# Kernel optimization log

Measured on AMD Instinct MI355X. Metric: run time of the kernel, lower is better.

## Reference

```python
import jax, jax.numpy as jnp
import numpy as np

H = 1024          # hidden_size
D = 4             # num_domains
B, S = 8, 2048


def setup_inputs() -> dict:
    key = jax.random.key(0)
    ks = jax.random.split(key, 12)
    inp = {
        "sequence_embeddings": jax.random.normal(ks[0], (B, S, H), jnp.float32),
        "volatility": jax.random.uniform(ks[1], (B, S, 1), jnp.float32) * 0.02 + 0.005,
        "risk_factors": jax.random.normal(ks[2], (B, S, 1), jnp.float32) * 0.01,
        # learned parameters (match torch init scales)
        "domain_feature_weights": jax.random.normal(ks[3], (H, 2 * H), jnp.float32) * 0.02,
        "domain_feature_bias": jnp.zeros((2 * H,), jnp.float32),
        "domain_classifier_weights": jax.random.normal(ks[4], (2 * H, D), jnp.float32) * 0.02,
        "domain_classifier_bias": jnp.zeros((D,), jnp.float32),
        "volatility_router_weights": jax.random.normal(ks[5], (1, 8, D), jnp.float32) * 0.1,
        "volatility_router_bias": jnp.zeros((8, D), jnp.float32),
        "risk_router_weights": jax.random.normal(ks[6], (1, 8, D), jnp.float32) * 0.1,
        "risk_router_bias": jnp.zeros((8, D), jnp.float32),
        "stats_router_weights": jax.random.normal(ks[7], (3, 12, D), jnp.float32) * 0.1,
        "stats_router_bias": jnp.zeros((12, D), jnp.float32),
        "expert_weights": jax.random.normal(ks[8], (D, 2 * H, H), jnp.float32) * 0.02,
        "expert_bias": jnp.zeros((D, H), jnp.float32),
    }
    return inp


def reference(sequence_embeddings, volatility, risk_factors,
              domain_feature_weights, domain_feature_bias,
              domain_classifier_weights, domain_classifier_bias,
              volatility_router_weights, volatility_router_bias,
              risk_router_weights, risk_router_bias,
              stats_router_weights, stats_router_bias,
              expert_weights, expert_bias):
    x = sequence_embeddings
    # shared domain feature extractor: [B,S,H] -> [B,S,2H]
    feat = jnp.tanh(jnp.einsum('bsh,hf->bsf', x, domain_feature_weights) + domain_feature_bias)
    # content-based domain logits [B,S,D]
    dom_logits = jnp.einsum('bsf,fd->bsd', feat, domain_classifier_weights) + domain_classifier_bias
    # volatility router: scalar -> 8 hidden units per domain, tanh, sum -> [B,S,D]
    vol_logits = jnp.tanh(volatility[..., None] * volatility_router_weights[0]
                          + volatility_router_bias).sum(axis=-2)
    # risk router, same structure
    risk_logits = jnp.tanh(risk_factors[..., None] * risk_router_weights[0]
                           + risk_router_bias).sum(axis=-2)
    # per-token statistics (mean/std/max over feature dim) -> [B,S,3]
    stats = jnp.stack([x.mean(axis=-1), x.std(axis=-1), x.max(axis=-1)], axis=-1)
    stats_logits = jnp.tanh(jnp.einsum('bsc,ckd->bskd', stats, stats_router_weights)
                            + stats_router_bias).sum(axis=-2)
    # combined routing distribution over domains
    routing_probs = jax.nn.softmax(dom_logits + vol_logits + risk_logits + stats_logits, axis=-1)
    # dispatch every token through all D experts: [B,S,D,H]
    expert_out = jnp.einsum('bsf,dfh->bsdh', feat, expert_weights) + expert_bias
    # gated combine: [B,S,H]
    out = jnp.einsum('bsd,bsdh->bsh', routing_probs, expert_out)
    return out
```

## Files before the change

kernel.cpp:

```cpp
#include <hip/hip_runtime.h>
#include <hip/hip_bf16.h>
#include <cstdint>
#include <cstddef>

typedef __bf16 bf16_t;
typedef bf16_t bf16x8 __attribute__((ext_vector_type(8)));
typedef bf16_t bf16x4 __attribute__((ext_vector_type(4)));
typedef float  f32x4  __attribute__((ext_vector_type(4)));
typedef int    i32x4  __attribute__((ext_vector_type(4)));

#define TOK 16384
#define Hh  1024
#define F2  2048
#define NC  4096

__device__ __forceinline__ void gload_lds16(const bf16_t* g, bf16_t* lds) {
  __builtin_amdgcn_global_load_lds(
      (const __attribute__((address_space(1))) void*)g,
      (__attribute__((address_space(3))) void*)lds, 16, 0, 0);
}
__device__ __forceinline__ void gload_lds16b(const int8_t* g, int8_t* lds) {
  __builtin_amdgcn_global_load_lds(
      (const __attribute__((address_space(1))) void*)g,
      (__attribute__((address_space(3))) void*)lds, 16, 0, 0);
}

__global__ __launch_bounds__(256)
void k_tr_wf(const float* __restrict__ in, bf16_t* __restrict__ out) {
  __shared__ float T[64][65];
  const int f0 = blockIdx.x * 64, h0 = blockIdx.y * 64;
  const int tid = threadIdx.x;
  const int c4 = (tid & 15) * 4, r = tid >> 4;
  #pragma unroll
  for (int p = 0; p < 4; ++p) {
    int hh = p * 16 + r;
    float4 v = *(const float4*)&in[(size_t)(h0 + hh) * F2 + f0 + c4];
    T[c4 + 0][hh] = v.x; T[c4 + 1][hh] = v.y; T[c4 + 2][hh] = v.z; T[c4 + 3][hh] = v.w;
  }
  __syncthreads();
  #pragma unroll
  for (int p = 0; p < 4; ++p) {
    int ff = p * 16 + r;
    bf16x4 o = { (bf16_t)T[ff][c4 + 0], (bf16_t)T[ff][c4 + 1],
                 (bf16_t)T[ff][c4 + 2], (bf16_t)T[ff][c4 + 3] };
    *(bf16x4*)&out[(size_t)(f0 + ff) * Hh + h0 + c4] = o;
  }
}

__global__ void k_we_scale1(const float* __restrict__ We, float* __restrict__ pmax) {
  int ht = blockIdx.x, fc = blockIdx.y, d = blockIdx.z;
  int h = ht * 256 + threadIdx.x;
  float m = 0.f;
  for (int ff = 0; ff < 256; ++ff) {
    float v = We[((size_t)d * F2 + fc * 256 + ff) * Hh + h];
    m = fmaxf(m, fabsf(v));
  }
  pmax[(size_t)(h * 4 + d) * 8 + fc] = m;
}
__global__ void k_we_scale2(const float* __restrict__ pmax, float* __restrict__ SB) {
  int cp = blockIdx.x * 256 + threadIdx.x;
  float m = 0.f;
  #pragma unroll
  for (int i = 0; i < 8; ++i) m = fmaxf(m, pmax[(size_t)cp * 8 + i]);
  SB[cp] = m;
}

__global__ __launch_bounds__(256)
void k_tr_we(const float* __restrict__ in, const float* __restrict__ SB,
             int8_t* __restrict__ out) {
  __shared__ float T[64][65];
  const int f0 = blockIdx.x * 64, h0 = blockIdx.y * 64, d = blockIdx.z;
  const float* ind = in + (size_t)d * F2 * Hh;
  const int tid = threadIdx.x;
  const int c4 = (tid & 15) * 4, r = tid >> 4;
  #pragma unroll
  for (int p = 0; p < 4; ++p) {
    int ff = p * 16 + r;
    float4 v = *(const float4*)&ind[(size_t)(f0 + ff) * Hh + h0 + c4];
    T[c4 + 0][ff] = v.x; T[c4 + 1][ff] = v.y; T[c4 + 2][ff] = v.z; T[c4 + 3][ff] = v.w;
  }
  __syncthreads();
  #pragma unroll
  for (int p = 0; p < 4; ++p) {
    int hh = p * 16 + r;
    int cp = (h0 + hh) * 4 + d;
    float m = SB[cp];
    float inv = (m > 1e-30f) ? 127.f / m : 0.f;
    char4 o;
    o.x = (int8_t)__float2int_rn(T[hh][c4 + 0] * inv);
    o.y = (int8_t)__float2int_rn(T[hh][c4 + 1] * inv);
    o.z = (int8_t)__float2int_rn(T[hh][c4 + 2] * inv);
    o.w = (int8_t)__float2int_rn(T[hh][c4 + 3] * inv);
    *(char4*)&out[(size_t)cp * F2 + f0 + c4] = o;
  }
}

__global__ void k_router_w(const float* __restrict__ x, const float* __restrict__ vol,
                           const float* __restrict__ risk, const float* __restrict__ clsb,
                           const float* __restrict__ vw, const float* __restrict__ vb,
                           const float* __restrict__ rw, const float* __restrict__ rb,
                           const float* __restrict__ sw, const float* __restrict__ sb,
                           bf16_t* __restrict__ xbf, float* __restrict__ LP,
                           int m0, int Tc) {
  int w = threadIdx.x >> 6, l = threadIdx.x & 63;
  int t = blockIdx.x * 4 + w;
  if (t >= Tc) return;
  int s = m0 + t;
  const float4* xr = (const float4*)(x + (size_t)s * Hh);
  bf16x4* xo = (bf16x4*)(xbf + (size_t)s * Hh);
  float sum = 0.f, sq = 0.f, mx = -1e30f;
  #pragma unroll
  for (int it = 0; it < 4; ++it) {
    float4 v = xr[it * 64 + l];
    sum += v.x + v.y + v.z + v.w;
    sq  += v.x * v.x + v.y * v.y + v.z * v.z + v.w * v.w;
    mx = fmaxf(mx, fmaxf(fmaxf(v.x, v.y), fmaxf(v.z, v.w)));
    bf16x4 o = { (bf16_t)v.x, (bf16_t)v.y, (bf16_t)v.z, (bf16_t)v.w };
    xo[it * 64 + l] = o;
  }
  #pragma unroll
  for (int off = 32; off; off >>= 1) {
    sum += __shfl_xor(sum, off, 64);
    sq  += __shfl_xor(sq,  off, 64);
    mx   = fmaxf(mx, __shfl_xor(mx, off, 64));
  }
  if (l < 4) {
    int d = l;
    float mean = sum * (1.0f / Hh);
    float var  = sq * (1.0f / Hh) - mean * mean;
    float sd   = sqrtf(fmaxf(var, 0.f));
    float v = vol[s], rk = risk[s];
    float acc = clsb[d];
    #pragma unroll
    for (int k = 0; k < 8; ++k)  acc += tanhf(v  * vw[k*4+d] + vb[k*4+d]);
    #pragma unroll
    for (int k = 0; k < 8; ++k)  acc += tanhf(rk * rw[k*4+d] + rb[k*4+d]);
    #pragma unroll
    for (int k = 0; k < 12; ++k)
      acc += tanhf(mean * sw[k*4+d] + sd * sw[48 + k*4+d] + mx * sw[96 + k*4+d] + sb[k*4+d]);
    LP[t * 4 + d] = acc;
  }
}

__global__ void k_dom(const int8_t* __restrict__ feat, const float* __restrict__ Wc,
                      float* __restrict__ LP) {
  int w = threadIdx.x >> 6, l = threadIdx.x & 63;
  int t = blockIdx.x * 4 + w;
  const int8_t* fr = feat + (size_t)t * F2;
  const float4* Wc4 = (const float4*)Wc;
  float a0 = 0, a1 = 0, a2 = 0, a3 = 0;
  #pragma unroll
  for (int it = 0; it < 4; ++it) {
    int f0 = it * 512 + l * 8;
    int2 v = *(const int2*)(fr + f0);
    #pragma unroll
    for (int j = 0; j < 8; ++j) {
      int word = (j < 4) ? v.x : v.y;
      float vf = (float)((signed char)(word >> (8 * (j & 3)))) * (1.f / 127.f);
      float4 wv = Wc4[f0 + j];
      a0 += vf * wv.x; a1 += vf * wv.y; a2 += vf * wv.z; a3 += vf * wv.w;
    }
  }
  #pragma unroll
  for (int off = 32; off; off >>= 1) {
    a0 += __shfl_xor(a0, off, 64); a1 += __shfl_xor(a1, off, 64);
    a2 += __shfl_xor(a2, off, 64); a3 += __shfl_xor(a3, off, 64);
  }
  if (l == 0) {
    float l0 = a0 + LP[t*4+0], l1 = a1 + LP[t*4+1];
    float l2 = a2 + LP[t*4+2], l3 = a3 + LP[t*4+3];
    float m = fmaxf(fmaxf(l0, l1), fmaxf(l2, l3));
    float e0 = expf(l0 - m), e1 = expf(l1 - m), e2 = expf(l2 - m), e3 = expf(l3 - m);
    float inv = 1.f / (e0 + e1 + e2 + e3);
    LP[t*4+0] = e0 * inv; LP[t*4+1] = e1 * inv; LP[t*4+2] = e2 * inv; LP[t*4+3] = e3 * inv;
  }
}

__global__ __launch_bounds__(512, 1)
void k_feat_gemm256(const bf16_t* __restrict__ A, const bf16_t* __restrict__ Bt,
                    const float* __restrict__ bias, int8_t* __restrict__ feat, int nbm) {
  constexpr int K = Hh, NT = K / 32;
  __shared__ bf16_t lds[4 * 8192 * 2];
  bf16_t* ldsB = lds + 32768;
  const int tid = threadIdx.x;
  const int l = tid & 63, wid = tid >> 6;
  const int wm = wid >> 2, wn = wid & 3;
  const int l15 = l & 15, lg = l >> 4;

  const int nwg = nbm * 8, cpx = nwg >> 3;
  int swzb = (blockIdx.x & 7) * cpx + (blockIdx.x >> 3);
  const int bm = swzb % nbm, bn = swzb / nbm;

  const bf16_t* gA = A  + (size_t)(bm * 256) * K;
  const bf16_t* gB = Bt + (size_t)(bn * 256) * K;

  int s_row[2], s_gx[2];
  #pragma unroll
  for (int i = 0; i < 2; ++i) {
    int slot = i * 512 + tid;
    s_row[i] = slot >> 2;
    s_gx[i]  = ((slot & 3) ^ ((s_row[i] >> 1) & 3)) << 3;
  }

  #define GLOAD(g, ts) do {                                                   \
    if ((g) < 2)                                                              \
      gload_lds16(gA + (size_t)s_row[g] * K + (ts) * 32 + s_gx[g],            \
                  lds  + ((ts) & 3) * 8192 + ((g) * 512 + tid) * 8);          \
    else                                                                      \
      gload_lds16(gB + (size_t)s_row[(g)-2] * K + (ts) * 32 + s_gx[(g)-2],    \
                  ldsB + ((ts) & 3) * 8192 + (((g)-2) * 512 + tid) * 8);      \
  } while (0)
  #define FENCE asm volatile("" ::: "memory")
  #define SB0 __builtin_amdgcn_sched_barrier(0)

  const int cswz = ((lg ^ ((l15 >> 1) & 3)) << 3);
  f32x4 acc[8][4] = {};
  bf16x8 bE[4], aE[4], bO[4], aO[4], aH[4];

  #pragma unroll
  for (int g = 0; g < 4; ++g) GLOAD(g, 0);
  #pragma unroll
  for (int g = 0; g < 4; ++g) GLOAD(g, 1);
  #pragma unroll
  for (int g = 0; g < 4; ++g) GLOAD(g, 2);
  asm volatile("s_waitcnt vmcnt(4)" ::: "memory");
  FENCE; __builtin_amdgcn_s_barrier(); FENCE;
  #pragma unroll
  for (int ni = 0; ni < 4; ++ni)
    bE[ni] = *(const bf16x8*)&ldsB[(wn * 64 + ni * 16 + l15) * 32 + cswz];
  #pragma unroll
  for (int mi = 0; mi < 4; ++mi)
    aE[mi] = *(const bf16x8*)&lds[(wm * 128 + mi * 16 + l15) * 32 + cswz];

  #define MFMA8(q, f0, f1, bset)                                               \
    __builtin_amdgcn_s_setprio(1);                                             \
    _Pragma("unroll")                                                          \
    for (int ni = 0; ni < 4; ++ni) {                                           \
      acc[q][ni]   = __builtin_amdgcn_mfma_f32_16x16x32_bf16(f0, bset[ni], acc[q][ni],   0, 0, 0); \
      acc[q+1][ni] = __builtin_amdgcn_mfma_f32_16x16x32_bf16(f1, bset[ni], acc[q+1][ni], 0, 0, 0); \
    }                                                                          \
    __builtin_amdgcn_s_setprio(0)

  #define TILE(T, bC, aC, bN, aN, DOSTAGE, DOREADS, VMODE)                     \
  {                                                                            \
    const bf16_t* AsC = lds  + ((T) & 3) * 8192;                               \
    const bf16_t* AsN = lds  + (((T) + 1) & 3) * 8192;                         \
    const bf16_t* BsN = ldsB + (((T) + 1) & 3) * 8192;                         \
    if (DOSTAGE) GLOAD(0, (T) + 3);                                            \
    _Pragma("unroll")                                                          \
    for (int mi = 0; mi < 4; ++mi)                                             \
      aH[mi] = *(const bf16x8*)&AsC[(wm * 128 + 64 + mi * 16 + l15) * 32 + cswz]; \
    SB0;                                                                       \
    MFMA8(0, aC[0], aC[1], bC);                                                \
    SB0;                                                                       \
    if (DOSTAGE) GLOAD(1, (T) + 3);                                            \
    if (DOREADS) {                                                             \
      _Pragma("unroll")                                                        \
      for (int ni = 0; ni < 4; ++ni)                                           \
        bN[ni] = *(const bf16x8*)&BsN[(wn * 64 + ni * 16 + l15) * 32 + cswz];  \
    }                                                                          \
    SB0;                                                                       \
    MFMA8(2, aC[2], aC[3], bC);                                                \
    SB0;                                                                       \
    if (DOSTAGE) GLOAD(2, (T) + 3);                                            \
    if (DOREADS) {                                                             \
      _Pragma("unroll")                                                        \
      for (int mi = 0; mi < 4; ++mi)                                           \
        aN[mi] = *(const bf16x8*)&AsN[(wm * 128 + mi * 16 + l15) * 32 + cswz]; \
    }                                                                          \
    SB0;                                                                       \
    MFMA8(4, aH[0], aH[1], bC);                                                \
    SB0;                                                                       \
    if (VMODE == 1)      asm volatile("s_waitcnt vmcnt(3)" ::: "memory");      \
    else if (VMODE == 2) asm volatile("s_waitcnt vmcnt(0)" ::: "memory");      \
    if (DOSTAGE) GLOAD(3, (T) + 3);                                            \
    SB0;                                                                       \
    MFMA8(6, aH[2], aH[3], bC);                                                \
    FENCE; __builtin_amdgcn_s_barrier(); FENCE;                                \
  }

  for (int tp = 0; tp < NT - 4; tp += 2) {
    TILE(tp,     bE, aE, bO, aO, true, true, 1);
    TILE(tp + 1, bO, aO, bE, aE, true, true, 1);
  }
  TILE(NT - 4, bE, aE, bO, aO, true,  true,  1);
  TILE(NT - 3, bO, aO, bE, aE, false, true,  2);
  TILE(NT - 2, bE, aE, bO, aO, false, true,  0);
  TILE(NT - 1, bO, aO, bE, aE, false, false, 0);
  #undef TILE
  #undef MFMA8
  #undef GLOAD
  #undef FENCE
  #undef SB0

  #pragma unroll
  for (int ni = 0; ni < 4; ++ni) {
    int gn = bn * 256 + wn * 64 + ni * 16 + l15;
    float bv = bias[gn];
    #pragma unroll
    for (int mi = 0; mi < 8; ++mi) {
      int gmBase = bm * 256 + wm * 128 + mi * 16 + lg * 4;
      #pragma unroll
      for (int r = 0; r < 4; ++r) {
        float t = tanhf(acc[mi][ni][r] + bv);
        feat[(size_t)(gmBase + r) * F2 + gn] = (int8_t)__float2int_rn(t * 127.f);
      }
    }
  }
}

__global__ __launch_bounds__(512, 1)
void k_expert_gemm256(const int8_t* __restrict__ A, const int8_t* __restrict__ Bt,
                      const float* __restrict__ P, const float* __restrict__ EB,
                      const float* __restrict__ SBq, float* __restrict__ out, int nbm) {
  constexpr int K = F2, NT = K / 64;
  __shared__ int8_t lds[4 * 16384 * 2];
  int8_t* ldsB = lds + 65536;
  const int tid = threadIdx.x;
  const int l = tid & 63, wid = tid >> 6;
  const int wm = wid >> 2, wn = wid & 3;
  const int l15 = l & 15, lg = l >> 4;

  const int nwg = nbm * 16, cpx = nwg >> 3;
  int swzb = (blockIdx.x & 7) * cpx + (blockIdx.x >> 3);
  const int bm = swzb % nbm, bn = swzb / nbm;

  const int8_t* gA = A  + (size_t)(bm * 256) * K;
  const int8_t* gB = Bt + (size_t)(bn * 256) * K;

  int s_row[2], s_gxB[2];
  #pragma unroll
  for (int i = 0; i < 2; ++i) {
    int slot = i * 512 + tid;
    s_row[i]  = slot >> 2;
    s_gxB[i]  = ((slot & 3) ^ ((s_row[i] >> 1) & 3)) << 4;
  }

  #define GLOAD(g, ts) do {                                                   \
    if ((g) < 2)                                                              \
      gload_lds16b(gA + (size_t)s_row[g] * K + (ts) * 64 + s_gxB[g],          \
                   lds  + ((ts) & 3) * 16384 + ((g) * 512 + tid) * 16);       \
    else                                                                      \
      gload_lds16b(gB + (size_t)s_row[(g)-2] * K + (ts) * 64 + s_gxB[(g)-2],  \
                   ldsB + ((ts) & 3) * 16384 + (((g)-2) * 512 + tid) * 16);   \
  } while (0)
  #define FENCE asm volatile("" ::: "memory")
  #define SB0 __builtin_amdgcn_sched_barrier(0)

  const int cswzB = ((lg ^ ((l15 >> 1) & 3)) << 4);
  i32x4 acc[8][4] = {};
  i32x4 bE[4], aE[4], bO[4], aO[4], aH[4];

  #pragma unroll
  for (int g = 0; g < 4; ++g) GLOAD(g, 0);
  #pragma unroll
  for (int g = 0; g < 4; ++g) GLOAD(g, 1);
  #pragma unroll
  for (int g = 0; g < 4; ++g) GLOAD(g, 2);
  asm volatile("s_waitcnt vmcnt(4)" ::: "memory");
  FENCE; __builtin_amdgcn_s_barrier(); FENCE;
  #pragma unroll
  for (int ni = 0; ni < 4; ++ni)
    bE[ni] = *(const i32x4*)&ldsB[(wn * 64 + ni * 16 + l15) * 64 + cswzB];
  #pragma unroll
  for (int mi = 0; mi < 4; ++mi)
    aE[mi] = *(const i32x4*)&lds[(wm * 128 + mi * 16 + l15) * 64 + cswzB];

  #define MFMA8(q, f0, f1, bset)                                               \
    __builtin_amdgcn_s_setprio(1);                                             \
    _Pragma("unroll")                                                          \
    for (int ni = 0; ni < 4; ++ni) {                                           \
      acc[q][ni]   = __builtin_amdgcn_mfma_i32_16x16x64_i8(f0, bset[ni], acc[q][ni],   0, 0, 0); \
      acc[q+1][ni] = __builtin_amdgcn_mfma_i32_16x16x64_i8(f1, bset[ni], acc[q+1][ni], 0, 0, 0); \
    }                                                                          \
    __builtin_amdgcn_s_setprio(0)

  #define TILE(T, bC, aC, bN, aN, DOSTAGE, DOREADS, VMODE)                     \
  {                                                                            \
    const int8_t* AsC = lds  + ((T) & 3) * 16384;                              \
    const int8_t* AsN = lds  + (((T) + 1) & 3) * 16384;                        \
    const int8_t* BsN = ldsB + (((T) + 1) & 3) * 16384;                        \
    if (DOSTAGE) GLOAD(0, (T) + 3);                                            \
    _Pragma("unroll")                                                          \
    for (int mi = 0; mi < 4; ++mi)                                             \
      aH[mi] = *(const i32x4*)&AsC[(wm * 128 + 64 + mi * 16 + l15) * 64 + cswzB]; \
    SB0;                                                                       \
    MFMA8(0, aC[0], aC[1], bC);                                                \
    SB0;                                                                       \
    if (DOSTAGE) GLOAD(1, (T) + 3);                                            \
    if (DOREADS) {                                                             \
      _Pragma("unroll")                                                        \
      for (int ni = 0; ni < 4; ++ni)                                           \
        bN[ni] = *(const i32x4*)&BsN[(wn * 64 + ni * 16 + l15) * 64 + cswzB];  \
    }                                                                          \
    SB0;                                                                       \
    MFMA8(2, aC[2], aC[3], bC);                                                \
    SB0;                                                                       \
    if (DOSTAGE) GLOAD(2, (T) + 3);                                            \
    if (DOREADS) {                                                             \
      _Pragma("unroll")                                                        \
      for (int mi = 0; mi < 4; ++mi)                                           \
        aN[mi] = *(const i32x4*)&AsN[(wm * 128 + mi * 16 + l15) * 64 + cswzB]; \
    }                                                                          \
    SB0;                                                                       \
    MFMA8(4, aH[0], aH[1], bC);                                                \
    SB0;                                                                       \
    if (VMODE == 1)      asm volatile("s_waitcnt vmcnt(3)" ::: "memory");      \
    else if (VMODE == 2) asm volatile("s_waitcnt vmcnt(0)" ::: "memory");      \
    if (DOSTAGE) GLOAD(3, (T) + 3);                                            \
    SB0;                                                                       \
    MFMA8(6, aH[2], aH[3], bC);                                                \
    FENCE; __builtin_amdgcn_s_barrier(); FENCE;                                \
  }

  for (int tp = 0; tp < NT - 4; tp += 2) {
    TILE(tp,     bE, aE, bO, aO, true, true, 1);
    TILE(tp + 1, bO, aO, bE, aE, true, true, 1);
  }
  TILE(NT - 4, bE, aE, bO, aO, true,  true,  1);
  TILE(NT - 3, bO, aO, bE, aE, false, true,  2);
  TILE(NT - 2, bE, aE, bO, aO, false, true,  0);
  TILE(NT - 1, bO, aO, bE, aE, false, false, 0);
  #undef TILE
  #undef MFMA8
  #undef GLOAD
  #undef FENCE
  #undef SB0

  #pragma unroll
  for (int mi = 0; mi < 8; ++mi) {
    int gmBase = bm * 256 + wm * 128 + mi * 16 + lg * 4;
    float pr[4];
    #pragma unroll
    for (int r = 0; r < 4; ++r) pr[r] = P[(gmBase + r) * 4 + (l & 3)];
    #pragma unroll
    for (int ni = 0; ni < 4; ++ni) {
      int colp = bn * 256 + wn * 64 + ni * 16 + l15;
      int h = colp >> 2;
      float dq = SBq[colp] * (1.0f / 16129.0f);
      #pragma unroll
      for (int r = 0; r < 4; ++r) {
        float sv = (float)acc[mi][ni][r] * dq * pr[r];
        sv += __shfl_xor(sv, 1, 64);
        sv += __shfl_xor(sv, 2, 64);
        if ((l & 3) == 0) {
          int gm = gmBase + r;
          float bt = P[gm*4+0]*EB[h] + P[gm*4+1]*EB[Hh+h]
                   + P[gm*4+2]*EB[2*Hh+h] + P[gm*4+3]*EB[3*Hh+h];
          out[(size_t)gm * Hh + h] = sv + bt;
        }
      }
    }
  }
}

extern "C" void kernel_launch(void* const* d_in, const int* in_sizes, int n_in,
                              void* d_out, int out_size, void* d_ws, size_t ws_size,
                              hipStream_t stream) {
  const float *x  = (const float*)d_in[0],  *vol = (const float*)d_in[1];
  const float *risk = (const float*)d_in[2], *Wf = (const float*)d_in[3];
  const float *fb = (const float*)d_in[4],  *Wc = (const float*)d_in[5];
  const float *cb = (const float*)d_in[6],  *vw = (const float*)d_in[7];
  const float *vb = (const float*)d_in[8],  *rw = (const float*)d_in[9];
  const float *rb = (const float*)d_in[10], *sw = (const float*)d_in[11];
  const float *sb = (const float*)d_in[12], *We = (const float*)d_in[13];
  const float *eb = (const float*)d_in[14];

  float* out = (float*)d_out;
  char* ws = (char*)d_ws;
  const size_t KB = 1024, MB = 1024 * 1024;

  float*  LP     = (float*) ws;
  float*  SBq    = (float*) (ws + 256 * KB);
  float*  pmax   = (float*) (ws + 512 * KB);
  bf16_t* wft    = (bf16_t*)(ws + 1 * MB);
  int8_t* wet    = (int8_t*)(ws + 5 * MB);
  bf16_t* xbf    = (bf16_t*)(ws + 13 * MB);
  const size_t base = 45 * MB;
  int Tc = TOK;
  while (Tc > 1024 && base + (size_t)Tc * F2 > ws_size) Tc >>= 1;
  int8_t* feat = (int8_t*)(ws + base);

  k_tr_wf    <<<dim3(F2 / 64, Hh / 64), 256, 0, stream>>>(Wf, wft);
  k_we_scale1<<<dim3(4, 8, 4), 256, 0, stream>>>(We, pmax);
  k_we_scale2<<<16, 256, 0, stream>>>(pmax, SBq);
  k_tr_we    <<<dim3(F2 / 64, Hh / 64, 4), 256, 0, stream>>>(We, SBq, wet);

  for (int m0 = 0; m0 < TOK; m0 += Tc) {
    k_router_w<<<Tc / 4, 256, 0, stream>>>(
        x, vol, risk, cb, vw, vb, rw, rb, sw, sb, xbf, LP, m0, Tc);
    int nbmF = Tc / 256;
    k_feat_gemm256<<<nbmF * (F2 / 256), 512, 0, stream>>>(
        xbf + (size_t)m0 * Hh, wft, fb, feat, nbmF);
    k_dom<<<Tc / 4, 256, 0, stream>>>(feat, Wc, LP);
    k_expert_gemm256<<<nbmF * (NC / 256), 512, 0, stream>>>(
        feat, wet, LP, eb, SBq, out + (size_t)m0 * Hh, nbmF);
  }
}
```

Baseline: 487.9 us.

## Shrink GEMM tiles to 256x128 with simple double-buffered loop for occupancy

Both GEMM kernels change from 256x256 tiles with a hand-scheduled 4-stage LDS pipeline to 256x128 tiles. They now use a plain 2-stage double buffer, a 4x2 wave layout and a full vmcnt(0) wait each iteration. Launch bounds rise to allow 4 workgroups per CU, and the grid doubles. The aim is to hide latency through occupancy rather than explicit software pipelining, at the cost of lower arithmetic intensity per tile and losing the interleaved load/MFMA schedule.

```diff
diff --git a/kernel.cpp b/kernel.cpp
--- a/kernel.cpp
+++ b/kernel.cpp
@@ -176,266 +176,172 @@
   }
 }
 
-__global__ __launch_bounds__(512, 1)
+__global__ __launch_bounds__(512, 4)
 void k_feat_gemm256(const bf16_t* __restrict__ A, const bf16_t* __restrict__ Bt,
                     const float* __restrict__ bias, int8_t* __restrict__ feat, int nbm) {
   constexpr int K = Hh, NT = K / 32;
-  __shared__ bf16_t lds[4 * 8192 * 2];
-  bf16_t* ldsB = lds + 32768;
+  __shared__ bf16_t lds[2 * 8192 + 2 * 4096];
+  bf16_t* ldsB = lds + 16384;
   const int tid = threadIdx.x;
   const int l = tid & 63, wid = tid >> 6;
-  const int wm = wid >> 2, wn = wid & 3;
+  const int wm = wid >> 1, wn = wid & 1;
   const int l15 = l & 15, lg = l >> 4;
 
-  const int nwg = nbm * 8, cpx = nwg >> 3;
+  const int nwg = nbm * 16, cpx = nwg >> 3;
   int swzb = (blockIdx.x & 7) * cpx + (blockIdx.x >> 3);
   const int bm = swzb % nbm, bn = swzb / nbm;
 
   const bf16_t* gA = A  + (size_t)(bm * 256) * K;
-  const bf16_t* gB = Bt + (size_t)(bn * 256) * K;
-
-  int s_row[2], s_gx[2];
+  const bf16_t* gB = Bt + (size_t)(bn * 128) * K;
+
+  int aRow[2], aGx[2];
   #pragma unroll
   for (int i = 0; i < 2; ++i) {
     int slot = i * 512 + tid;
-    s_row[i] = slot >> 2;
-    s_gx[i]  = ((slot & 3) ^ ((s_row[i] >> 1) & 3)) << 3;
-  }
-
-  #define GLOAD(g, ts) do {                                                   \
-    if ((g) < 2)                                                              \
-      gload_lds16(gA + (size_t)s_row[g] * K + (ts) * 32 + s_gx[g],            \
-                  lds  + ((ts) & 3) * 8192 + ((g) * 512 + tid) * 8);          \
-    else                                                                      \
-      gload_lds16(gB + (size_t)s_row[(g)-2] * K + (ts) * 32 + s_gx[(g)-2],    \
-                  ldsB + ((ts) & 3) * 8192 + (((g)-2) * 512 + tid) * 8);      \
+    aRow[i] = slot >> 2;
+    aGx[i]  = ((slot & 3) ^ ((aRow[i] >> 1) & 3)) << 3;
+  }
+  const int bRow = tid >> 2;
+  const int bGx  = ((tid & 3) ^ ((bRow >> 1) & 3)) << 3;
+
+  #define STAGE(ts) do {                                                       \
+    int b_ = (ts) & 1;                                                         \
+    _Pragma("unroll")                                                          \
+    for (int i = 0; i < 2; ++i)                                                \
+      gload_lds16(gA + (size_t)aRow[i] * K + (ts) * 32 + aGx[i],               \
+                  lds + b_ * 8192 + (i * 512 + tid) * 8);                      \
+    gload_lds16(gB + (size_t)bRow * K + (ts) * 32 + bGx,                       \
+                ldsB + b_ * 4096 + tid * 8);                                   \
   } while (0)
   #define FENCE asm volatile("" ::: "memory")
-  #define SB0 __builtin_amdgcn_sched_barrier(0)
 
   const int cswz = ((lg ^ ((l15 >> 1) & 3)) << 3);
-  f32x4 acc[8][4] = {};
-  bf16x8 bE[4], aE[4], bO[4], aO[4], aH[4];
-
-  #pragma unroll
-  for (int g = 0; g < 4; ++g) GLOAD(g, 0);
-  #pragma unroll
-  for (int g = 0; g < 4; ++g) GLOAD(g, 1);
-  #pragma unroll
-  for (int g = 0; g < 4; ++g) GLOAD(g, 2);
-  asm volatile("s_waitcnt vmcnt(4)" ::: "memory");
+  f32x4 acc[4][4] = {};
+
+  STAGE(0);
+  asm volatile("s_waitcnt vmcnt(0)" ::: "memory");
   FENCE; __builtin_amdgcn_s_barrier(); FENCE;
-  #pragma unroll
-  for (int ni = 0; ni < 4; ++ni)
-    bE[ni] = *(const bf16x8*)&ldsB[(wn * 64 + ni * 16 + l15) * 32 + cswz];
-  #pragma unroll
-  for (int mi = 0; mi < 4; ++mi)
-    aE[mi] = *(const bf16x8*)&lds[(wm * 128 + mi * 16 + l15) * 32 + cswz];
-
-  #define MFMA8(q, f0, f1, bset)                                               \
-    __builtin_amdgcn_s_setprio(1);                                             \
-    _Pragma("unroll")                                                          \
-    for (int ni = 0; ni < 4; ++ni) {                                           \
-      acc[q][ni]   = __builtin_amdgcn_mfma_f32_16x16x32_bf16(f0, bset[ni], acc[q][ni],   0, 0, 0); \
-      acc[q+1][ni] = __builtin_amdgcn_mfma_f32_16x16x32_bf16(f1, bset[ni], acc[q+1][ni], 0, 0, 0); \
-    }                                                                          \
-    __builtin_amdgcn_s_setprio(0)
-
-  #define TILE(T, bC, aC, bN, aN, DOSTAGE, DOREADS, VMODE)                     \
-  {                                                                            \
-    const bf16_t* AsC = lds  + ((T) & 3) * 8192;                               \
-    const bf16_t* AsN = lds  + (((T) + 1) & 3) * 8192;                         \
-    const bf16_t* BsN = ldsB + (((T) + 1) & 3) * 8192;                         \
-    if (DOSTAGE) GLOAD(0, (T) + 3);                                            \
-    _Pragma("unroll")                                                          \
-    for (int mi = 0; mi < 4; ++mi)                                             \
-      aH[mi] = *(const bf16x8*)&AsC[(wm * 128 + 64 + mi * 16 + l15) * 32 + cswz]; \
-    SB0;                                                                       \
-    MFMA8(0, aC[0], aC[1], bC);                                                \
-    SB0;                                                                       \
-    if (DOSTAGE) GLOAD(1, (T) + 3);                                            \
-    if (DOREADS) {                                                             \
-      _Pragma("unroll")                                                        \
-      for (int ni = 0; ni < 4; ++ni)                                           \
-        bN[ni] = *(const bf16x8*)&BsN[(wn * 64 + ni * 16 + l15) * 32 + cswz];  \
-    }                                                                          \
-    SB0;                                                                       \
-    MFMA8(2, aC[2], aC[3], bC);                                                \
-    SB0;                                                                       \
-    if (DOSTAGE) GLOAD(2, (T) + 3);                                            \
-    if (DOREADS) {                                                             \
-      _Pragma("unroll")                                                        \
-      for (int mi = 0; mi < 4; ++mi)                                           \
-        aN[mi] = *(const bf16x8*)&AsN[(wm * 128 + mi * 16 + l15) * 32 + cswz]; \
-    }                                                                          \
-    SB0;                                                                       \
-    MFMA8(4, aH[0], aH[1], bC);                                                \
-    SB0;                                                                       \
-    if (VMODE == 1)      asm volatile("s_waitcnt vmcnt(3)" ::: "memory");      \
-    else if (VMODE == 2) asm volatile("s_waitcnt vmcnt(0)" ::: "memory");      \
-    if (DOSTAGE) GLOAD(3, (T) + 3);                                            \
-    SB0;                                                                       \
-    MFMA8(6, aH[2], aH[3], bC);                                                \
-    FENCE; __builtin_amdgcn_s_barrier(); FENCE;                                \
-  }
-
-  for (int tp = 0; tp < NT - 4; tp += 2) {
-    TILE(tp,     bE, aE, bO, aO, true, true, 1);
-    TILE(tp + 1, bO, aO, bE, aE, true, true, 1);
-  }
-  TILE(NT - 4, bE, aE, bO, aO, true,  true,  1);
-  TILE(NT - 3, bO, aO, bE, aE, false, true,  2);
-  TILE(NT - 2, bE, aE, bO, aO, false, true,  0);
-  TILE(NT - 1, bO, aO, bE, aE, false, false, 0);
-  #undef TILE
-  #undef MFMA8
-  #undef GLOAD
+
+  for (int t = 0; t < NT; ++t) {
+    const bf16_t* As_ = lds  + (t & 1) * 8192;
+    const bf16_t* Bs_ = ldsB + (t & 1) * 4096;
+    if (t + 1 < NT) STAGE(t + 1);
+    bf16x8 af[4], bf[4];
+    #pragma unroll
+    for (int ni = 0; ni < 4; ++ni)
+      bf[ni] = *(const bf16x8*)&Bs_[(wn * 64 + ni * 16 + l15) * 32 + cswz];
+    #pragma unroll
+    for (int mi = 0; mi < 4; ++mi)
+      af[mi] = *(const bf16x8*)&As_[(wm * 64 + mi * 16 + l15) * 32 + cswz];
+    __builtin_amdgcn_s_setprio(1);
+    #pragma unroll
+    for (int ni = 0; ni < 4; ++ni)
+      #pragma unroll
+      for (int mi = 0; mi < 4; ++mi)
+        acc[mi][ni] = __builtin_amdgcn_mfma_f32_16x16x32_bf16(af[mi], bf[ni], acc[mi][ni], 0, 0, 0);
+    __builtin_amdgcn_s_setprio(0);
+    asm volatile("s_waitcnt vmcnt(0)" ::: "memory");
+    FENCE; __builtin_amdgcn_s_barrier(); FENCE;
+  }
+  #undef STAGE
   #undef FENCE
-  #undef SB0
 
   #pragma unroll
   for (int ni = 0; ni < 4; ++ni) {
-    int gn = bn * 256 + wn * 64 + ni * 16 + l15;
+    int gn = bn * 128 + wn * 64 + ni * 16 + l15;
     float bv = bias[gn];
     #pragma unroll
-    for (int mi = 0; mi < 8; ++mi) {
-      int gmBase = bm * 256 + wm * 128 + mi * 16 + lg * 4;
+    for (int mi = 0; mi < 4; ++mi) {
+      int gmBase = bm * 256 + wm * 64 + mi * 16 + lg * 4;
       #pragma unroll
       for (int r = 0; r < 4; ++r) {
-        float t = tanhf(acc[mi][ni][r] + bv);
-        feat[(size_t)(gmBase + r) * F2 + gn] = (int8_t)__float2int_rn(t * 127.f);
+        float tv = tanhf(acc[mi][ni][r] + bv);
+        feat[(size_t)(gmBase + r) * F2 + gn] = (int8_t)__float2int_rn(tv * 127.f);
       }
     }
   }
 }
 
-__global__ __launch_bounds__(512, 1)
+__global__ __launch_bounds__(512, 4)
 void k_expert_gemm256(const int8_t* __restrict__ A, const int8_t* __restrict__ Bt,
                       const float* __restrict__ P, const float* __restrict__ EB,
                       const float* __restrict__ SBq, float* __restrict__ out, int nbm) {
   constexpr int K = F2, NT = K / 64;
-  __shared__ int8_t lds[4 * 16384 * 2];
-  int8_t* ldsB = lds + 65536;
+  __shared__ int8_t lds[2 * 16384 + 2 * 8192];
+  int8_t* ldsB = lds + 32768;
   const int tid = threadIdx.x;
   const int l = tid & 63, wid = tid >> 6;
-  const int wm = wid >> 2, wn = wid & 3;
+  const int wm = wid >> 1, wn = wid & 1;
   const int l15 = l & 15, lg = l >> 4;
 
-  const int nwg = nbm * 16, cpx = nwg >> 3;
+  const int nwg = nbm * 32, cpx = nwg >> 3;
   int swzb = (blockIdx.x & 7) * cpx + (blockIdx.x >> 3);
   const int bm = swzb % nbm, bn = swzb / nbm;
 
   const int8_t* gA = A  + (size_t)(bm * 256) * K;
-  const int8_t* gB = Bt + (size_t)(bn * 256) * K;
-
-  int s_row[2], s_gxB[2];
+  const int8_t* gB = Bt + (size_t)(bn * 128) * K;
+
+  int aRow[2], aGx[2];
   #pragma unroll
   for (int i = 0; i < 2; ++i) {
     int slot = i * 512 + tid;
-    s_row[i]  = slot >> 2;
-    s_gxB[i]  = ((slot & 3) ^ ((s_row[i] >> 1) & 3)) << 4;
-  }
-
-  #define GLOAD(g, ts) do {                                                   \
-    if ((g) < 2)                                                              \
-      gload_lds16b(gA + (size_t)s_row[g] * K + (ts) * 64 + s_gxB[g],          \
-                   lds  + ((ts) & 3) * 16384 + ((g) * 512 + tid) * 16);       \
-    else                                                                      \
-      gload_lds16b(gB + (size_t)s_row[(g)-2] * K + (ts) * 64 + s_gxB[(g)-2],  \
-                   ldsB + ((ts) & 3) * 16384 + (((g)-2) * 512 + tid) * 16);   \
+    aRow[i] = slot >> 2;
+    aGx[i]  = ((slot & 3) ^ ((aRow[i] >> 1) & 3)) << 4;
+  }
+  const int bRow = tid >> 2;
+  const int bGx  = ((tid & 3) ^ ((bRow >> 1) & 3)) << 4;
+
+  #define STAGE(ts) do {                                                       \
+    int b_ = (ts) & 1;                                                         \
+    _Pragma("unroll")                                                          \
+    for (int i = 0; i < 2; ++i)                                                \
+      gload_lds16b(gA + (size_t)aRow[i] * K + (ts) * 64 + aGx[i],              \
+                   lds + b_ * 16384 + (i * 512 + tid) * 16);                   \
+    gload_lds16b(gB + (size_t)bRow * K + (ts) * 64 + bGx,                      \
+                 ldsB + b_ * 8192 + tid * 16);                                 \
   } while (0)
   #define FENCE asm volatile("" ::: "memory")
-  #define SB0 __builtin_amdgcn_sched_barrier(0)
 
   const int cswzB = ((lg ^ ((l15 >> 1) & 3)) << 4);
-  i32x4 acc[8][4] = {};
-  i32x4 bE[4], aE[4], bO[4], aO[4], aH[4];
-
-  #pragma unroll
-  for (int g = 0; g < 4; ++g) GLOAD(g, 0);
-  #pragma unroll
-  for (int g = 0; g < 4; ++g) GLOAD(g, 1);
-  #pragma unroll
-  for (int g = 0; g < 4; ++g) GLOAD(g, 2);
-  asm volatile("s_waitcnt vmcnt(4)" ::: "memory");
+  i32x4 acc[4][4] = {};
+
+  STAGE(0);
+  asm volatile("s_waitcnt vmcnt(0)" ::: "memory");
   FENCE; __builtin_amdgcn_s_barrier(); FENCE;
-  #pragma unroll
-  for (int ni = 0; ni < 4; ++ni)
-    bE[ni] = *(const i32x4*)&ldsB[(wn * 64 + ni * 16 + l15) * 64 + cswzB];
-  #pragma unroll
-  for (int mi = 0; mi < 4; ++mi)
-    aE[mi] = *(const i32x4*)&lds[(wm * 128 + mi * 16 + l15) * 64 + cswzB];
-
-  #define MFMA8(q, f0, f1, bset)                                               \
-    __builtin_amdgcn_s_setprio(1);                                             \
-    _Pragma("unroll")                                                          \
-    for (int ni = 0; ni < 4; ++ni) {                                           \
-      acc[q][ni]   = __builtin_amdgcn_mfma_i32_16x16x64_i8(f0, bset[ni], acc[q][ni],   0, 0, 0); \
-      acc[q+1][ni] = __builtin_amdgcn_mfma_i32_16x16x64_i8(f1, bset[ni], acc[q+1][ni], 0, 0, 0); \
-    }                                                                          \
-    __builtin_amdgcn_s_setprio(0)
-
-  #define TILE(T, bC, aC, bN, aN, DOSTAGE, DOREADS, VMODE)                     \
-  {                                                                            \
-    const int8_t* AsC = lds  + ((T) & 3) * 16384;                              \
-    const int8_t* AsN = lds  + (((T) + 1) & 3) * 16384;                        \
-    const int8_t* BsN = ldsB + (((T) + 1) & 3) * 16384;                        \
-    if (DOSTAGE) GLOAD(0, (T) + 3);                                            \
-    _Pragma("unroll")                                                          \
-    for (int mi = 0; mi < 4; ++mi)                                             \
-      aH[mi] = *(const i32x4*)&AsC[(wm * 128 + 64 + mi * 16 + l15) * 64 + cswzB]; \
-    SB0;                                                                       \
-    MFMA8(0, aC[0], aC[1], bC);                                                \
-    SB0;                                                                       \
-    if (DOSTAGE) GLOAD(1, (T) + 3);                                            \
-    if (DOREADS) {                                                             \
-      _Pragma("unroll")                                                        \
-      for (int ni = 0; ni < 4; ++ni)                                           \
-        bN[ni] = *(const i32x4*)&BsN[(wn * 64 + ni * 16 + l15) * 64 + cswzB];  \
-    }                                                                          \
-    SB0;                                                                       \
-    MFMA8(2, aC[2], aC[3], bC);                                                \
-    SB0;                                                                       \
-    if (DOSTAGE) GLOAD(2, (T) + 3);                                            \
-    if (DOREADS) {                                                             \
-      _Pragma("unroll")                                                        \
-      for (int mi = 0; mi < 4; ++mi)                                           \
-        aN[mi] = *(const i32x4*)&AsN[(wm * 128 + mi * 16 + l15) * 64 + cswzB]; \
-    }                                                                          \
-    SB0;                                                                       \
-    MFMA8(4, aH[0], aH[1], bC);                                                \
-    SB0;                                                                       \
-    if (VMODE == 1)      asm volatile("s_waitcnt vmcnt(3)" ::: "memory");      \
-    else if (VMODE == 2) asm volatile("s_waitcnt vmcnt(0)" ::: "memory");      \
-    if (DOSTAGE) GLOAD(3, (T) + 3);                                            \
-    SB0;                                                                       \
-    MFMA8(6, aH[2], aH[3], bC);                                                \
-    FENCE; __builtin_amdgcn_s_barrier(); FENCE;                                \
-  }
-
-  for (int tp = 0; tp < NT - 4; tp += 2) {
-    TILE(tp,     bE, aE, bO, aO, true, true, 1);
-    TILE(tp + 1, bO, aO, bE, aE, true, true, 1);
-  }
-  TILE(NT - 4, bE, aE, bO, aO, true,  true,  1);
-  TILE(NT - 3, bO, aO, bE, aE, false, true,  2);
-  TILE(NT - 2, bE, aE, bO, aO, false, true,  0);
-  TILE(NT - 1, bO, aO, bE, aE, false, false, 0);
-  #undef TILE
-  #undef MFMA8
-  #undef GLOAD
+
+  for (int t = 0; t < NT; ++t) {
+    const int8_t* As_ = lds  + (t & 1) * 16384;
+    const int8_t* Bs_ = ldsB + (t & 1) * 8192;
+    if (t + 1 < NT) STAGE(t + 1);
+    i32x4 af[4], bf[4];
+    #pragma unroll
+    for (int ni = 0; ni < 4; ++ni)
+      bf[ni] = *(const i32x4*)&Bs_[(wn * 64 + ni * 16 + l15) * 64 + cswzB];
+    #pragma unroll
+    for (int mi = 0; mi < 4; ++mi)
+      af[mi] = *(const i32x4*)&As_[(wm * 64 + mi * 16 + l15) * 64 + cswzB];
+    __builtin_amdgcn_s_setprio(1);
+    #pragma unroll
+    for (int ni = 0; ni < 4; ++ni)
+      #pragma unroll
+      for (int mi = 0; mi < 4; ++mi)
+        acc[mi][ni] = __builtin_amdgcn_mfma_i32_16x16x64_i8(af[mi], bf[ni], acc[mi][ni], 0, 0, 0);
+    __builtin_amdgcn_s_setprio(0);
+    asm volatile("s_waitcnt vmcnt(0)" ::: "memory");
+    FENCE; __builtin_amdgcn_s_barrier(); FENCE;
+  }
+  #undef STAGE
   #undef FENCE
-  #undef SB0
-
-  #pragma unroll
-  for (int mi = 0; mi < 8; ++mi) {
-    int gmBase = bm * 256 + wm * 128 + mi * 16 + lg * 4;
+
+  #pragma unroll
+  for (int mi = 0; mi < 4; ++mi) {
+    int gmBase = bm * 256 + wm * 64 + mi * 16 + lg * 4;
     float pr[4];
     #pragma unroll
     for (int r = 0; r < 4; ++r) pr[r] = P[(gmBase + r) * 4 + (l & 3)];
     #pragma unroll
     for (int ni = 0; ni < 4; ++ni) {
-      int colp = bn * 256 + wn * 64 + ni * 16 + l15;
+      int colp = bn * 128 + wn * 64 + ni * 16 + l15;
       int h = colp >> 2;
       float dq = SBq[colp] * (1.0f / 16129.0f);
       #pragma unroll
@@ -490,10 +396,10 @@
     k_router_w<<<Tc / 4, 256, 0, stream>>>(
         x, vol, risk, cb, vw, vb, rw, rb, sw, sb, xbf, LP, m0, Tc);
     int nbmF = Tc / 256;
-    k_feat_gemm256<<<nbmF * (F2 / 256), 512, 0, stream>>>(
+    k_feat_gemm256<<<nbmF * (F2 / 128), 512, 0, stream>>>(
         xbf + (size_t)m0 * Hh, wft, fb, feat, nbmF);
     k_dom<<<Tc / 4, 256, 0, stream>>>(feat, Wc, LP);
-    k_expert_gemm256<<<nbmF * (NC / 256), 512, 0, stream>>>(
+    k_expert_gemm256<<<nbmF * (NC / 128), 512, 0, stream>>>(
         feat, wet, LP, eb, SBq, out + (size_t)m0 * Hh, nbmF);
   }
 }
```

Measured after the change: 475.9 us. 1.03x faster.
